# Kernel tuning notes

Hardware: AMD Instinct MI355X
Metric: run time of the kernel (lower is better)

## Reference

```python
import jax, jax.numpy as jnp
import numpy as np

B, T = 512, 16384


def ema(x, alpha):
    """Row-wise EMA: y_0 = x_0, y_t = alpha*x_t + (1-alpha)*y_{t-1}. x: [B, T]."""
    one_minus = 1.0 - alpha

    def step(carry, xt):  # carry: [B], xt: [B]
        y = alpha * xt + one_minus * carry
        return y, y

    init = x[:, 0]
    _, ys = jax.lax.scan(step, init, x[:, 1:].T)  # ys: [T-1, B]
    return jnp.concatenate([x[:, :1], ys.T], axis=1)  # [B, T]


def setup_inputs() -> dict:
    key = jax.random.key(0)
    data = jax.random.normal(key, (B, T), dtype=jnp.float32)
    return {"data": data, "short_period": 12, "long_period": 26, "signal_period": 9}


def reference(data, short_period, long_period, signal_period):
    short_alpha = 2.0 / (short_period + 1)
    long_alpha = 2.0 / (long_period + 1)
    signal_alpha = 2.0 / (signal_period + 1)
    macd_line = ema(data, short_alpha) - ema(data, long_alpha)
    signal_line = ema(macd_line, signal_alpha)
    hist = macd_line - signal_line
    return (macd_line, signal_line, hist)
```

## Files before the change

### kernel.cpp

```cpp
#include <hip/hip_runtime.h>


constexpr int kB = 512;
constexpr int kT = 16384;
constexpr int kSeg = 1024;
constexpr int kWarm = 256;
constexpr int kChunk = 256;
constexpr int kSegsPerRow = kT / kSeg;
constexpr int kWavesPerBlock = 4;

struct Ema {
  float a, b, b2, b3, b4;
  float m[6];
  float pw;
};

__device__ __forceinline__ Ema make_ema(float a, int lane) {
  Ema e;
  e.a  = a;
  e.b  = 1.0f - a;
  e.b2 = e.b * e.b;
  e.b3 = e.b2 * e.b;
  e.b4 = e.b2 * e.b2;
  float m  = e.b4;
  float pw = 1.0f;
#pragma unroll
  for (int i = 0; i < 6; ++i) {
    e.m[i] = m;
    if (lane & (1 << i)) pw *= m;
    m = m * m;
  }
  e.pw = pw;
  return e;
}

__device__ __forceinline__ void ema_chunk(const Ema& c, int lane,
                                          float x0, float x1, float x2, float x3,
                                          float& carry,
                                          float& y0, float& y1, float& y2, float& y3) {
  float l0 = c.a * x0;
  float l1 = fmaf(c.b, l0, c.a * x1);
  float l2 = fmaf(c.b, l1, c.a * x2);
  float l3 = fmaf(c.b, l2, c.a * x3);
  float z = l3;
#pragma unroll
  for (int i = 0; i < 6; ++i) {
    const int d = 1 << i;
    float t = __shfl_up(z, d, 64);
    if (lane >= d) z = fmaf(c.m[i], t, z);
  }
  float ex = __shfl_up(z, 1, 64);
  if (lane == 0) ex = 0.0f;
  const float cin = fmaf(c.pw, carry, ex);
  y0 = fmaf(c.b,  cin, l0);
  y1 = fmaf(c.b2, cin, l1);
  y2 = fmaf(c.b3, cin, l2);
  y3 = fmaf(c.b4, cin, l3);
  carry = __shfl(y3, 63, 64);
}

__global__ __launch_bounds__(kWavesPerBlock * 64, 4)
void macd_kernel(const float* __restrict__ x,
                 const int* __restrict__ p_short,
                 const int* __restrict__ p_long,
                 const int* __restrict__ p_sig,
                 float* __restrict__ out) {
  const int lane    = threadIdx.x & 63;
  const int wave    = threadIdx.x >> 6;
  const int wave_id = blockIdx.x * kWavesPerBlock + wave;
  const int row     = wave_id / kSegsPerRow;
  const int seg     = wave_id % kSegsPerRow;
  const int s       = seg * kSeg;

  const Ema cs = make_ema(2.0f / (float)(p_short[0] + 1), lane);
  const Ema cl = make_ema(2.0f / (float)(p_long[0]  + 1), lane);
  const Ema cg = make_ema(2.0f / (float)(p_sig[0]   + 1), lane);

  const int p0      = (seg == 0) ? 0 : (s - kWarm);
  const int nwarm   = (seg == 0) ? 0 : (kWarm / kChunk);
  const int nchunks = nwarm + kSeg / kChunk;

  const int rowbase = row * kT;
  const float* xseg = x + rowbase + p0;

  const float x_init = xseg[0];
  float c_s = x_init, c_l = x_init, c_g = 0.0f;

  float* om = out + rowbase;
  float* og = out + kB * kT + rowbase;
  float* oh = out + 2 * kB * kT + rowbase;

  for (int ch = 0; ch < nchunks; ++ch) {
    const int off = ch * kChunk + lane * 4;
    const float4 xv = *(const float4*)(xseg + off);

    float s0, s1, s2, s3, l0, l1, l2, l3;
    ema_chunk(cs, lane, xv.x, xv.y, xv.z, xv.w, c_s, s0, s1, s2, s3);
    ema_chunk(cl, lane, xv.x, xv.y, xv.z, xv.w, c_l, l0, l1, l2, l3);

    const float m0 = s0 - l0, m1 = s1 - l1, m2 = s2 - l2, m3 = s3 - l3;

    float g0, g1, g2, g3;
    ema_chunk(cg, lane, m0, m1, m2, m3, c_g, g0, g1, g2, g3);

    if (ch >= nwarm) {
      const int pos = p0 + off;
      float4 mv; mv.x = m0; mv.y = m1; mv.z = m2; mv.w = m3;
      float4 gv; gv.x = g0; gv.y = g1; gv.z = g2; gv.w = g3;
      float4 hv; hv.x = m0 - g0; hv.y = m1 - g1; hv.z = m2 - g2; hv.w = m3 - g3;
      *(float4*)(om + pos) = mv;
      *(float4*)(og + pos) = gv;
      *(float4*)(oh + pos) = hv;
    }
  }
}

extern "C" void kernel_launch(void* const* d_in, const int* in_sizes, int n_in,
                              void* d_out, int out_size, void* d_ws, size_t ws_size,
                              hipStream_t stream) {
  const float* x  = (const float*)d_in[0];
  const int* ps   = (const int*)d_in[1];
  const int* pl   = (const int*)d_in[2];
  const int* pg   = (const int*)d_in[3];
  float* out      = (float*)d_out;

  const int total_waves = kB * kSegsPerRow;
  const int blocks = total_waves / kWavesPerBlock;
  macd_kernel<<<blocks, kWavesPerBlock * 64, 0, stream>>>(x, ps, pl, pg, out);
}
```

Before: 135.4 us.

## Replace chunked wave scans with per-lane serial EMA plus one wave scan

Each lane now loads 20 contiguous elements covering the warm-up window plus the segment. It runs the short and long EMAs serially in registers, then joins lanes with a single shuffle-based carry scan per EMA. Before, each of five 256-element chunks needed three full wave scans. The aim is to cut shuffle count and serial scan latency. In exchange, per-lane stores are strided rather than fully coalesced float4 runs, and register pressure rises. Segment 0 now clamps negative indices to x[0], relying on the decay over the warm-up span to match the exact initial condition.

Result: slower. 145.7 us (+7.6%).

```diff
diff --git a/kernel.cpp b/kernel.cpp
--- a/kernel.cpp
+++ b/kernel.cpp
@@ -5,58 +5,27 @@
 constexpr int kT = 16384;
 constexpr int kSeg = 1024;
 constexpr int kWarm = 256;
-constexpr int kChunk = 256;
+constexpr int kE = 20;
 constexpr int kSegsPerRow = kT / kSeg;
 constexpr int kWavesPerBlock = 4;
 
-struct Ema {
-  float a, b, b2, b3, b4;
-  float m[6];
-  float pw;
-};
-
-__device__ __forceinline__ Ema make_ema(float a, int lane) {
-  Ema e;
-  e.a  = a;
-  e.b  = 1.0f - a;
-  e.b2 = e.b * e.b;
-  e.b3 = e.b2 * e.b;
-  e.b4 = e.b2 * e.b2;
-  float m  = e.b4;
-  float pw = 1.0f;
-#pragma unroll
-  for (int i = 0; i < 6; ++i) {
-    e.m[i] = m;
-    if (lane & (1 << i)) pw *= m;
-    m = m * m;
-  }
-  e.pw = pw;
-  return e;
-}
-
-__device__ __forceinline__ void ema_chunk(const Ema& c, int lane,
-                                          float x0, float x1, float x2, float x3,
-                                          float& carry,
-                                          float& y0, float& y1, float& y2, float& y3) {
-  float l0 = c.a * x0;
-  float l1 = fmaf(c.b, l0, c.a * x1);
-  float l2 = fmaf(c.b, l1, c.a * x2);
-  float l3 = fmaf(c.b, l2, c.a * x3);
-  float z = l3;
+__device__ __forceinline__ float wave_scan_carry(float agg, float M, int lane) {
+  float m = M;
+  float z = agg;
 #pragma unroll
   for (int i = 0; i < 6; ++i) {
     const int d = 1 << i;
     float t = __shfl_up(z, d, 64);
-    if (lane >= d) z = fmaf(c.m[i], t, z);
+    if (lane >= d) z = fmaf(m, t, z);
+    m = m * m;
   }
   float ex = __shfl_up(z, 1, 64);
-  if (lane == 0) ex = 0.0f;
-  const float cin = fmaf(c.pw, carry, ex);
-  y0 = fmaf(c.b,  cin, l0);
-  y1 = fmaf(c.b2, cin, l1);
-  y2 = fmaf(c.b3, cin, l2);
-  y3 = fmaf(c.b4, cin, l3);
-  carry = __shfl(y3, 63, 64);
+  return (lane == 0) ? 0.0f : ex;
+}
+
+__device__ __forceinline__ float pow20(float b) {
+  float b2 = b * b, b4 = b2 * b2, b8 = b4 * b4, b16 = b8 * b8;
+  return b16 * b4;
 }
 
 __global__ __launch_bounds__(kWavesPerBlock * 64, 4)
@@ -66,48 +35,74 @@
                  const int* __restrict__ p_sig,
                  float* __restrict__ out) {
   const int lane    = threadIdx.x & 63;
-  const int wave    = threadIdx.x >> 6;
-  const int wave_id = blockIdx.x * kWavesPerBlock + wave;
+  const int wave_id = (blockIdx.x * blockDim.x + threadIdx.x) >> 6;
   const int row     = wave_id / kSegsPerRow;
   const int seg     = wave_id % kSegsPerRow;
-  const int s       = seg * kSeg;
+  const int s0      = seg * kSeg;
 
-  const Ema cs = make_ema(2.0f / (float)(p_short[0] + 1), lane);
-  const Ema cl = make_ema(2.0f / (float)(p_long[0]  + 1), lane);
-  const Ema cg = make_ema(2.0f / (float)(p_sig[0]   + 1), lane);
+  const float a_s = 2.0f / (float)(p_short[0] + 1), b_s = 1.0f - a_s;
+  const float a_l = 2.0f / (float)(p_long[0]  + 1), b_l = 1.0f - a_l;
+  const float a_g = 2.0f / (float)(p_sig[0]   + 1), b_g = 1.0f - a_g;
 
-  const int p0      = (seg == 0) ? 0 : (s - kWarm);
-  const int nwarm   = (seg == 0) ? 0 : (kWarm / kChunk);
-  const int nchunks = nwarm + kSeg / kChunk;
+  const float* xr = x + row * kT;
+  const int base = s0 - kWarm + lane * kE;
 
-  const int rowbase = row * kT;
-  const float* xseg = x + rowbase + p0;
+  float xv[kE];
+  if (base >= 0) {
+#pragma unroll
+    for (int j = 0; j < kE / 4; ++j) {
+      const float4 v = *(const float4*)(xr + base + 4 * j);
+      xv[4 * j + 0] = v.x; xv[4 * j + 1] = v.y;
+      xv[4 * j + 2] = v.z; xv[4 * j + 3] = v.w;
+    }
+  } else {
+#pragma unroll
+    for (int i = 0; i < kE; ++i) {
+      const int p = base + i;
+      xv[i] = xr[p < 0 ? 0 : p];
+    }
+  }
 
-  const float x_init = xseg[0];
-  float c_s = x_init, c_l = x_init, c_g = 0.0f;
+  float ts = a_s * xv[0], tl = a_l * xv[0];
+#pragma unroll
+  for (int i = 1; i < kE; ++i) {
+    ts = fmaf(b_s, ts, a_s * xv[i]);
+    tl = fmaf(b_l, tl, a_l * xv[i]);
+  }
+  float cs = wave_scan_carry(ts, pow20(b_s), lane);
+  float cl = wave_scan_carry(tl, pow20(b_l), lane);
 
-  float* om = out + rowbase;
-  float* og = out + kB * kT + rowbase;
-  float* oh = out + 2 * kB * kT + rowbase;
+  float m[kE];
+#pragma unroll
+  for (int i = 0; i < kE; ++i) {
+    cs = fmaf(b_s, cs, a_s * xv[i]);
+    cl = fmaf(b_l, cl, a_l * xv[i]);
+    m[i] = cs - cl;
+  }
 
-  for (int ch = 0; ch < nchunks; ++ch) {
-    const int off = ch * kChunk + lane * 4;
-    const float4 xv = *(const float4*)(xseg + off);
+  float tg = a_g * m[0];
+#pragma unroll
+  for (int i = 1; i < kE; ++i) tg = fmaf(b_g, tg, a_g * m[i]);
+  float cg = wave_scan_carry(tg, pow20(b_g), lane);
 
-    float s0, s1, s2, s3, l0, l1, l2, l3;
-    ema_chunk(cs, lane, xv.x, xv.y, xv.z, xv.w, c_s, s0, s1, s2, s3);
-    ema_chunk(cl, lane, xv.x, xv.y, xv.z, xv.w, c_l, l0, l1, l2, l3);
+  float* om = out + row * kT;
+  float* og = om + kB * kT;
+  float* oh = og + kB * kT;
 
-    const float m0 = s0 - l0, m1 = s1 - l1, m2 = s2 - l2, m3 = s3 - l3;
-
-    float g0, g1, g2, g3;
-    ema_chunk(cg, lane, m0, m1, m2, m3, c_g, g0, g1, g2, g3);
-
-    if (ch >= nwarm) {
-      const int pos = p0 + off;
-      float4 mv; mv.x = m0; mv.y = m1; mv.z = m2; mv.w = m3;
-      float4 gv; gv.x = g0; gv.y = g1; gv.z = g2; gv.w = g3;
-      float4 hv; hv.x = m0 - g0; hv.y = m1 - g1; hv.z = m2 - g2; hv.w = m3 - g3;
+#pragma unroll
+  for (int j = 0; j < kE / 4; ++j) {
+    float4 mv, gv, hv;
+    mv.x = m[4 * j + 0]; mv.y = m[4 * j + 1];
+    mv.z = m[4 * j + 2]; mv.w = m[4 * j + 3];
+    cg = fmaf(b_g, cg, a_g * mv.x); gv.x = cg;
+    cg = fmaf(b_g, cg, a_g * mv.y); gv.y = cg;
+    cg = fmaf(b_g, cg, a_g * mv.z); gv.z = cg;
+    cg = fmaf(b_g, cg, a_g * mv.w); gv.w = cg;
+    const int e = lane * kE + 4 * j;
+    if (e >= kWarm) {
+      const int pos = s0 - kWarm + e;
+      hv.x = mv.x - gv.x; hv.y = mv.y - gv.y;
+      hv.z = mv.z - gv.z; hv.w = mv.w - gv.w;
       *(float4*)(om + pos) = mv;
       *(float4*)(og + pos) = gv;
       *(float4*)(oh + pos) = hv;
@@ -118,11 +113,11 @@
 extern "C" void kernel_launch(void* const* d_in, const int* in_sizes, int n_in,
                               void* d_out, int out_size, void* d_ws, size_t ws_size,
                               hipStream_t stream) {
-  const float* x  = (const float*)d_in[0];
-  const int* ps   = (const int*)d_in[1];
-  const int* pl   = (const int*)d_in[2];
-  const int* pg   = (const int*)d_in[3];
-  float* out      = (float*)d_out;
+  const float* x = (const float*)d_in[0];
+  const int* ps  = (const int*)d_in[1];
+  const int* pl  = (const int*)d_in[2];
+  const int* pg  = (const int*)d_in[3];
+  float* out     = (float*)d_out;
 
   const int total_waves = kB * kSegsPerRow;
   const int blocks = total_waves / kWavesPerBlock;
```
